# Optimization experiments

Hardware: AMD Instinct MI355X
Metric: run time of the kernel (lower is better)

Reference implementation:

```python
import jax, jax.numpy as jnp
import numpy as np

B, IN, H, CTX = 16384, 1024, 1024, 2048


def setup_inputs() -> dict:
    key = jax.random.key(0)
    ks = jax.random.split(key, 20)
    stdv = 1.0 / np.sqrt(H)
    u = lambda k, shape: jax.random.uniform(k, shape, jnp.float32, -stdv, stdv)
    inp = {
        "y": jax.random.normal(ks[0], (B, IN), jnp.float32),
        "ctx": jax.random.normal(ks[1], (B, CTX), jnp.float32),
        "c0": jax.random.normal(ks[2], (B, H), jnp.float32),
        "h0": jax.random.normal(ks[3], (B, H), jnp.float32),
        # Concatenated gate weights in order (i, f, o, c), matching the
        # per-gate matrices Wi..Wc, Ui..Uc, Ci..Cc of the original module.
        "W": u(ks[4], (4 * H, IN)),   # input projections
        "U": u(ks[5], (4 * H, H)),    # hidden projections
        "C": u(ks[6], (4 * H, CTX)),  # context projections
        "b": u(ks[7], (4 * H,)),      # gate biases
    }
    return inp


def reference(y, ctx, c0, h0, W, U, C, b):
    # One fused GEMM per input stream instead of 12 small ones; same math.
    gates = y @ W.T + h0 @ U.T + ctx @ C.T + b  # [B, 4H]
    gi, gf, go, gc = jnp.split(gates, 4, axis=-1)
    i = jax.nn.sigmoid(gi)
    f = jax.nn.sigmoid(gf)
    o = jax.nn.sigmoid(go)
    c_hat = jnp.tanh(gc)
    c = i * c_hat + f * c0
    h = o * jnp.tanh(c)
    return (c, h)
```

## Files before the change

kernel.cpp:

```cpp
#include <hip/hip_runtime.h>
#include <hip/hip_bf16.h>
#include <stdint.h>

typedef __attribute__((ext_vector_type(8))) short short8;
typedef __attribute__((ext_vector_type(8))) unsigned short ushort8;
typedef __attribute__((ext_vector_type(4))) float f32x4;
typedef __attribute__((ext_vector_type(8))) __bf16 bf16x8;

#define GAS __attribute__((address_space(1)))
#define LAS __attribute__((address_space(3)))

static constexpr int Bn = 16384;
static constexpr int Hn = 1024;
static constexpr int KT = 4096;
static constexpr int NT = KT / 64;

#define SBAR()   __builtin_amdgcn_s_barrier()
#define VMCNT(n) asm volatile("s_waitcnt vmcnt(" #n ")" ::: "memory")
#define FENCE()  asm volatile("" ::: "memory")

__device__ __forceinline__ unsigned short f2bf(float f) {
  unsigned u = __builtin_bit_cast(unsigned, f);
  u = (u + 0x7FFFu + ((u >> 16) & 1u)) >> 16;
  return (unsigned short)u;
}

__device__ __forceinline__ float fast_sigm(float x) {
  return __builtin_amdgcn_rcpf(1.f + __expf(-x));
}
__device__ __forceinline__ float fast_tanh(float x) {
  return 1.f - 2.f * __builtin_amdgcn_rcpf(__expf(2.f * x) + 1.f);
}

__global__ __launch_bounds__(256) void cvt_concat_k(
    const float* __restrict__ s0, const float* __restrict__ s1,
    const float* __restrict__ s2, unsigned short* __restrict__ dst,
    long long n8) {
  long long stride = (long long)gridDim.x * blockDim.x;
  for (long long g = (long long)blockIdx.x * blockDim.x + threadIdx.x; g < n8;
       g += stride) {
    long long row = g >> 9;
    int cg = (int)(g & 511) << 3;
    const float* src;
    if (cg < 1024)      src = s0 + row * 1024 + cg;
    else if (cg < 2048) src = s1 + row * 1024 + (cg - 1024);
    else                src = s2 + row * 2048 + (cg - 2048);
    float4 f0 = *(const float4*)src;
    float4 f1 = *(const float4*)(src + 4);
    ushort8 o;
    o[0] = f2bf(f0.x); o[1] = f2bf(f0.y); o[2] = f2bf(f0.z); o[3] = f2bf(f0.w);
    o[4] = f2bf(f1.x); o[5] = f2bf(f1.y); o[6] = f2bf(f1.z); o[7] = f2bf(f1.w);
    *(ushort8*)(dst + (g << 3)) = o;
  }
}

__global__ __launch_bounds__(512, 2) void lstm_gemm(
    const unsigned short* __restrict__ X, const unsigned short* __restrict__ Wc,
    const float* __restrict__ bias, const float* __restrict__ c0,
    float* __restrict__ out_c, float* __restrict__ out_h) {
  extern __shared__ char smem[];

  int bid = blockIdx.x;
  int swz = (bid & 7) * 128 + (bid >> 3);
  int mblk = swz & 63, cblk = swz >> 6;
  int brow0 = mblk * 256;
  int hcol0 = cblk * 64;

  int tid = threadIdx.x;
  int lane = tid & 63, wid = tid >> 6;
  int wr = wid >> 2, wc = wid & 3;

  const char* Xc = (const char*)X;
  const char* Wcc = (const char*)Wc;

  int rr = tid >> 3;
  uint32_t cbyte = (uint32_t)(((tid & 7) * 16) ^ ((rr & 7) << 4));
  uint32_t aoffj[4];
#pragma unroll
  for (int j = 0; j < 4; ++j)
    aoffj[j] = (uint32_t)(brow0 + j * 64 + rr) * (KT * 2) + cbyte;

  auto stage_A = [&](int tt, int dbuf) {
    int ts = tt < NT ? tt : NT - 1;
#pragma unroll
    for (int j = 0; j < 4; ++j) {
      const char* src = Xc + aoffj[j] + (uint32_t)ts * 128u;
      char* dst = smem + dbuf * 32768 + j * 8192 + wid * 1024;
      __builtin_amdgcn_global_load_lds((const GAS unsigned int*)src,
                                       (LAS unsigned int*)dst, 16, 0, 0);
    }
  };

  int kg = (lane >> 4) << 4;
  int sw = (lane & 7) << 4;
  int koff0 = kg ^ sw;
  int koff1 = (64 + kg) ^ sw;
  int fr = lane & 15;

  const char* bbp[4];
#pragma unroll
  for (int n = 0; n < 4; ++n) {
    int wrow = n * 1024 + hcol0 + wc * 16 + fr;
    bbp[n] = Wcc + (size_t)wrow * (KT * 2) + ((lane >> 4) << 4);
  }

  f32x4 acc[8][4] = {};
  short8 bfrE[4][2], bfrO[4][2];

  stage_A(0, 0);
  FENCE();
#pragma unroll
  for (int n = 0; n < 4; ++n) {
    bfrE[n][0] = *(const short8*)(bbp[n]);
    bfrE[n][1] = *(const short8*)(bbp[n] + 64);
  }
  stage_A(1, 1);

  int bufA = 0;

#define TILE(T_, BC, BN)                                                      \
  {                                                                           \
    VMCNT(12);                                                                \
    SBAR();                                                                   \
    int pb = bufA * 32768;                                                    \
    int stg = bufA + 2; if (stg >= 3) stg -= 3;                               \
    _Pragma("unroll")                                                         \
    for (int q = 0; q < 4; ++q) {                                             \
      int ab = pb + ((2 * q + wr) * 32 + fr) * 128;                           \
      short8 a0 = *(const short8*)(smem + ab + koff0);                        \
      short8 a1 = *(const short8*)(smem + ab + koff1);                        \
      short8 a2 = *(const short8*)(smem + ab + 2048 + koff0);                 \
      short8 a3 = *(const short8*)(smem + ab + 2048 + koff1);                 \
      if (q == 1) {                \
        int ts = (T_) + 1 < NT ? (T_) + 1 : NT - 1;                           \
        _Pragma("unroll")                                                     \
        for (int n = 0; n < 4; ++n) {                                         \
          BN[n][0] = *(const short8*)(bbp[n] + (size_t)ts * 128);             \
          BN[n][1] = *(const short8*)(bbp[n] + (size_t)ts * 128 + 64);        \
        }                                                                     \
      }                                                                       \
      if (q == 3) stage_A((T_) + 2, stg);                                     \
      __builtin_amdgcn_s_setprio(1);                                          \
      _Pragma("unroll")                                                       \
      for (int n = 0; n < 4; ++n) {                                           \
        acc[2 * q][n] = __builtin_amdgcn_mfma_f32_16x16x32_bf16(              \
            __builtin_bit_cast(bf16x8, a0), __builtin_bit_cast(bf16x8, BC[n][0]),\
            acc[2 * q][n], 0, 0, 0);                                          \
        acc[2 * q + 1][n] = __builtin_amdgcn_mfma_f32_16x16x32_bf16(          \
            __builtin_bit_cast(bf16x8, a2), __builtin_bit_cast(bf16x8, BC[n][0]),\
            acc[2 * q + 1][n], 0, 0, 0);                                      \
      }                                                                       \
      _Pragma("unroll")                                                       \
      for (int n = 0; n < 4; ++n) {                                           \
        acc[2 * q][n] = __builtin_amdgcn_mfma_f32_16x16x32_bf16(              \
            __builtin_bit_cast(bf16x8, a1), __builtin_bit_cast(bf16x8, BC[n][1]),\
            acc[2 * q][n], 0, 0, 0);                                          \
        acc[2 * q + 1][n] = __builtin_amdgcn_mfma_f32_16x16x32_bf16(          \
            __builtin_bit_cast(bf16x8, a3), __builtin_bit_cast(bf16x8, BC[n][1]),\
            acc[2 * q + 1][n], 0, 0, 0);                                      \
      }                                                                       \
      __builtin_amdgcn_s_setprio(0);                                          \
    }                                                                         \
    bufA = bufA + 1; if (bufA >= 3) bufA = 0;                                 \
  }

  for (int t = 0; t < NT; t += 2) {
    TILE(t, bfrE, bfrO)
    TILE(t + 1, bfrO, bfrE)
  }
#undef TILE

  int col = hcol0 + wc * 16 + fr;
  float bi = bias[col], bf_ = bias[1024 + col];
  float bo = bias[2048 + col], bc = bias[3072 + col];
#pragma unroll
  for (int m = 0; m < 8; ++m) {
    int row0 = brow0 + (2 * (m >> 1) + wr) * 32 + (m & 1) * 16 + ((lane >> 4) << 2);
#pragma unroll
    for (int j = 0; j < 4; ++j) {
      size_t idx = (size_t)(row0 + j) * 1024 + col;
      float i_ = fast_sigm(acc[m][0][j] + bi);
      float f_ = fast_sigm(acc[m][1][j] + bf_);
      float o_ = fast_sigm(acc[m][2][j] + bo);
      float ch = fast_tanh(acc[m][3][j] + bc);
      float cn = i_ * ch + f_ * c0[idx];
      out_c[idx] = cn;
      out_h[idx] = o_ * fast_tanh(cn);
    }
  }
}

__global__ __launch_bounds__(256) void lstm_naive(
    const float* __restrict__ y, const float* __restrict__ ctx,
    const float* __restrict__ c0, const float* __restrict__ h0,
    const float* __restrict__ W, const float* __restrict__ U,
    const float* __restrict__ C, const float* __restrict__ b,
    float* __restrict__ out_c, float* __restrict__ out_h) {
  size_t t = (size_t)blockIdx.x * blockDim.x + threadIdx.x;
  if (t >= (size_t)Bn * Hn) return;
  int row = (int)(t >> 10), col = (int)(t & 1023);
  float g[4];
#pragma unroll
  for (int gg = 0; gg < 4; ++gg) {
    int wrow = gg * 1024 + col;
    float s = b[wrow];
    const float* yr = y + (size_t)row * 1024;
    const float* Wr = W + (size_t)wrow * 1024;
    for (int k = 0; k < 1024; ++k) s += yr[k] * Wr[k];
    const float* hr = h0 + (size_t)row * 1024;
    const float* Ur = U + (size_t)wrow * 1024;
    for (int k = 0; k < 1024; ++k) s += hr[k] * Ur[k];
    const float* cr = ctx + (size_t)row * 2048;
    const float* Cr = C + (size_t)wrow * 2048;
    for (int k = 0; k < 2048; ++k) s += cr[k] * Cr[k];
    g[gg] = s;
  }
  float i_ = fast_sigm(g[0]), f_ = fast_sigm(g[1]);
  float o_ = fast_sigm(g[2]), ch = fast_tanh(g[3]);
  float cn = i_ * ch + f_ * c0[t];
  out_c[t] = cn;
  out_h[t] = o_ * fast_tanh(cn);
}

extern "C" void kernel_launch(void* const* d_in, const int* in_sizes, int n_in,
                              void* d_out, int out_size, void* d_ws, size_t ws_size,
                              hipStream_t stream) {
  const float* y   = (const float*)d_in[0];
  const float* ctx = (const float*)d_in[1];
  const float* c0  = (const float*)d_in[2];
  const float* h0  = (const float*)d_in[3];
  const float* W   = (const float*)d_in[4];
  const float* U   = (const float*)d_in[5];
  const float* C   = (const float*)d_in[6];
  const float* b   = (const float*)d_in[7];
  float* out = (float*)d_out;
  float* out_c = out;
  float* out_h = out + (size_t)Bn * Hn;

  const size_t needX = (size_t)Bn * KT * 2;
  const size_t needW = (size_t)(4 * Hn) * KT * 2;

  if (ws_size >= needX + needW) {
    unsigned short* Xb = (unsigned short*)d_ws;
    unsigned short* Wb = (unsigned short*)((char*)d_ws + needX);
    cvt_concat_k<<<2048, 256, 0, stream>>>(y, h0, ctx, Xb, (long long)Bn * 512);
    cvt_concat_k<<<2048, 256, 0, stream>>>(W, U, C, Wb, (long long)(4 * Hn) * 512);
    (void)hipFuncSetAttribute((const void*)lstm_gemm,
                              hipFuncAttributeMaxDynamicSharedMemorySize, 98304);
    lstm_gemm<<<1024, 512, 98304, stream>>>(Xb, Wb, b, c0, out_c, out_h);
  } else {
    lstm_naive<<<(Bn * Hn + 255) / 256, 256, 0, stream>>>(y, ctx, c0, h0, W, U, C,
                                                          b, out_c, out_h);
  }
}
```

Measured before the change: 694.6 us.

## Pack weights into MFMA fragment order and reorder block tile mapping

```diff
diff --git a/kernel.cpp b/kernel.cpp
--- a/kernel.cpp
+++ b/kernel.cpp
@@ -54,15 +54,40 @@
   }
 }
 
+__global__ __launch_bounds__(256) void cvt_pack_w(
+    const float* __restrict__ s0, const float* __restrict__ s1,
+    const float* __restrict__ s2, unsigned short* __restrict__ dst,
+    long long n8) {
+  long long stride = (long long)gridDim.x * blockDim.x;
+  for (long long g = (long long)blockIdx.x * blockDim.x + threadIdx.x; g < n8;
+       g += stride) {
+    long long row = g >> 9;
+    int cg = (int)(g & 511) << 3;
+    const float* src;
+    if (cg < 1024)      src = s0 + row * 1024 + cg;
+    else if (cg < 2048) src = s1 + row * 1024 + (cg - 1024);
+    else                src = s2 + row * 2048 + (cg - 2048);
+    float4 f0 = *(const float4*)src;
+    float4 f1 = *(const float4*)(src + 4);
+    ushort8 o;
+    o[0] = f2bf(f0.x); o[1] = f2bf(f0.y); o[2] = f2bf(f0.z); o[3] = f2bf(f0.w);
+    o[4] = f2bf(f1.x); o[5] = f2bf(f1.y); o[6] = f2bf(f1.z); o[7] = f2bf(f1.w);
+    int cb = (int)(row >> 4), fr = (int)(row & 15);
+    int k32 = cg >> 5, ksl = (cg >> 3) & 3;
+    long long off = ((long long)k32 * 256 + cb) * 512 + (fr + ksl * 16) * 8;
+    *(ushort8*)(dst + off) = o;
+  }
+}
+
 __global__ __launch_bounds__(512, 2) void lstm_gemm(
-    const unsigned short* __restrict__ X, const unsigned short* __restrict__ Wc,
+    const unsigned short* __restrict__ X, const unsigned short* __restrict__ Wp,
     const float* __restrict__ bias, const float* __restrict__ c0,
     float* __restrict__ out_c, float* __restrict__ out_h) {
   extern __shared__ char smem[];
 
   int bid = blockIdx.x;
   int swz = (bid & 7) * 128 + (bid >> 3);
-  int mblk = swz & 63, cblk = swz >> 6;
+  int mblk = swz >> 4, cblk = swz & 15;
   int brow0 = mblk * 256;
   int hcol0 = cblk * 64;
 
@@ -71,7 +96,7 @@
   int wr = wid >> 2, wc = wid & 3;
 
   const char* Xc = (const char*)X;
-  const char* Wcc = (const char*)Wc;
+  const char* Wpc = (const char*)Wp;
 
   int rr = tid >> 3;
   uint32_t cbyte = (uint32_t)(((tid & 7) * 16) ^ ((rr & 7) << 4));
@@ -100,8 +125,8 @@
   const char* bbp[4];
 #pragma unroll
   for (int n = 0; n < 4; ++n) {
-    int wrow = n * 1024 + hcol0 + wc * 16 + fr;
-    bbp[n] = Wcc + (size_t)wrow * (KT * 2) + ((lane >> 4) << 4);
+    int cb = n * 64 + cblk * 4 + wc;
+    bbp[n] = Wpc + ((size_t)cb * 64 + lane) * 16;
   }
 
   f32x4 acc[8][4] = {};
@@ -112,7 +137,7 @@
 #pragma unroll
   for (int n = 0; n < 4; ++n) {
     bfrE[n][0] = *(const short8*)(bbp[n]);
-    bfrE[n][1] = *(const short8*)(bbp[n] + 64);
+    bfrE[n][1] = *(const short8*)(bbp[n] + 262144);
   }
   stage_A(1, 1);
 
@@ -131,12 +156,13 @@
       short8 a1 = *(const short8*)(smem + ab + koff1);                        \
       short8 a2 = *(const short8*)(smem + ab + 2048 + koff0);                 \
       short8 a3 = *(const short8*)(smem + ab + 2048 + koff1);                 \
-      if (q == 1) {                \
+      if (q == 1) {          \
         int ts = (T_) + 1 < NT ? (T_) + 1 : NT - 1;                           \
+        size_t tb = (size_t)(2 * ts) * 262144u;                               \
         _Pragma("unroll")                                                     \
         for (int n = 0; n < 4; ++n) {                                         \
-          BN[n][0] = *(const short8*)(bbp[n] + (size_t)ts * 128);             \
-          BN[n][1] = *(const short8*)(bbp[n] + (size_t)ts * 128 + 64);        \
+          BN[n][0] = *(const short8*)(bbp[n] + tb);                           \
+          BN[n][1] = *(const short8*)(bbp[n] + tb + 262144);                  \
         }                                                                     \
       }                                                                       \
       if (q == 3) stage_A((T_) + 2, stg);                                     \
@@ -244,7 +270,7 @@
     unsigned short* Xb = (unsigned short*)d_ws;
     unsigned short* Wb = (unsigned short*)((char*)d_ws + needX);
     cvt_concat_k<<<2048, 256, 0, stream>>>(y, h0, ctx, Xb, (long long)Bn * 512);
-    cvt_concat_k<<<2048, 256, 0, stream>>>(W, U, C, Wb, (long long)(4 * Hn) * 512);
+    cvt_pack_w<<<2048, 256, 0, stream>>>(W, U, C, Wb, (long long)(4 * Hn) * 512);
     (void)hipFuncSetAttribute((const void*)lstm_gemm,
                               hipFuncAttributeMaxDynamicSharedMemorySize, 98304);
     lstm_gemm<<<1024, 512, 98304, stream>>>(Xb, Wb, b, c0, out_c, out_h);
```

Measured after the change: 585.6 us. -15.7%, faster.
